# Optimization experiments

Hardware: AMD Instinct MI355X
Metric: run time of the kernel (lower is better)

## Reference

```python
import jax, jax.numpy as jnp
import numpy as np

N = 50000
E = 800000
F_IN = 128
HID = 32
NEG_SLOPE = 0.2  # PyG GATConv default


def _gat_layer(x, src, dst, W, a_src, a_dst, b, heads, out_c, concat, n_nodes):
    # Linear transform per head: [N, heads, out_c]
    h = (x @ W).reshape(n_nodes, heads, out_c)
    # Per-node attention logits per head
    al_src = jnp.einsum('nhc,hc->nh', h, a_src)  # source contribution
    al_dst = jnp.einsum('nhc,hc->nh', h, a_dst)  # destination contribution
    # Edge logits (message j=src -> i=dst), leaky relu
    e = jax.nn.leaky_relu(al_src[src] + al_dst[dst], NEG_SLOPE)  # [E', heads]
    # Segment softmax over incoming edges of each destination node
    m = jax.ops.segment_max(e, dst, num_segments=n_nodes)
    ex = jnp.exp(e - m[dst])
    denom = jax.ops.segment_sum(ex, dst, num_segments=n_nodes)
    alpha = ex / denom[dst]  # [E', heads]; self-loops guarantee denom > 0
    # Weighted scatter-aggregate of source features
    msg = h[src] * alpha[:, :, None]  # [E', heads, out_c]
    out = jax.ops.segment_sum(msg, dst, num_segments=n_nodes)  # [N, heads, out_c]
    out = out.reshape(n_nodes, heads * out_c) if concat else out.mean(axis=1)
    return out + b


def setup_inputs() -> dict:
    key = jax.random.key(0)
    ks = jax.random.split(key, 10)
    x = jax.random.normal(ks[0], (N, F_IN), dtype=jnp.float32)
    edge_index = jax.random.randint(ks[1], (2, E), 0, N, dtype=jnp.int64)
    s = 0.1
    return {
        'x': x,
        'edge_index': edge_index,
        'W1': jax.random.normal(ks[2], (F_IN, 4 * HID), dtype=jnp.float32) * s,
        'a_src1': jax.random.normal(ks[3], (4, HID), dtype=jnp.float32) * s,
        'a_dst1': jax.random.normal(ks[4], (4, HID), dtype=jnp.float32) * s,
        'b1': jnp.zeros((4 * HID,), jnp.float32),
        'W2': jax.random.normal(ks[5], (4 * HID, 2 * HID), dtype=jnp.float32) * s,
        'a_src2': jax.random.normal(ks[6], (2, HID), dtype=jnp.float32) * s,
        'a_dst2': jax.random.normal(ks[7], (2, HID), dtype=jnp.float32) * s,
        'b2': jnp.zeros((2 * HID,), jnp.float32),
        'W3': jax.random.normal(ks[8], (2 * HID, 1), dtype=jnp.float32) * s,
        'a_src3': jax.random.normal(ks[9], (1, 1), dtype=jnp.float32) * s,
        'a_dst3': jax.random.normal(jax.random.fold_in(key, 99), (1, 1), dtype=jnp.float32) * s,
        'b3': jnp.zeros((1,), jnp.float32),
    }


def reference(x, edge_index, W1, a_src1, a_dst1, b1, W2, a_src2, a_dst2, b2, W3, a_src3, a_dst3, b3):
    n = x.shape[0]
    # add_self_loops=True (PyG default)
    loop = jnp.arange(n, dtype=edge_index.dtype)
    src = jnp.concatenate([edge_index[0], loop])
    dst = jnp.concatenate([edge_index[1], loop])
    h = _gat_layer(x, src, dst, W1, a_src1, a_dst1, b1, 4, HID, True, n)
    h = jax.nn.elu(h)  # dropout is identity in eval mode
    h = _gat_layer(h, src, dst, W2, a_src2, a_dst2, b2, 2, HID, True, n)
    h = jax.nn.elu(h)
    out = _gat_layer(h, src, dst, W3, a_src3, a_dst3, b3, 1, 1, False, n)
    return out  # [N, 1]
```

## Files before the change

### kernel.cpp

```cpp
#include <hip/hip_runtime.h>
#include <hip/hip_fp16.h>
#include <math.h>

#define F_IN 128
constexpr int SB = 256;
constexpr float LOG2E = 1.4426950408889634f;
constexpr int CAP = 131072;
constexpr int CHUNK = 2048;
constexpr int NPAD = 50176;

__global__ void scan1(const int* __restrict__ degr, int* __restrict__ out,
                      int* __restrict__ bsums, int n, int selfN) {
    __shared__ int sm[SB];
    int i = blockIdx.x * SB + threadIdx.x;
    int v = 0;
    if (i < n) {
#pragma unroll
        for (int r = 0; r < 8; ++r) v += degr[r * NPAD + i];
        if (i < selfN) v += 1;
    }
    sm[threadIdx.x] = v;
    __syncthreads();
    for (int d = 1; d < SB; d <<= 1) {
        int t = (threadIdx.x >= d) ? sm[threadIdx.x - d] : 0;
        __syncthreads();
        sm[threadIdx.x] += t;
        __syncthreads();
    }
    if (i < n) out[i] = sm[threadIdx.x] - v;
    if (threadIdx.x == SB - 1) bsums[blockIdx.x] = sm[SB - 1];
}

__global__ void scan2(int* __restrict__ bsums, int nb) {
    __shared__ int sm[SB];
    int v = (threadIdx.x < nb) ? bsums[threadIdx.x] : 0;
    sm[threadIdx.x] = v;
    __syncthreads();
    for (int d = 1; d < SB; d <<= 1) {
        int t = (threadIdx.x >= d) ? sm[threadIdx.x - d] : 0;
        __syncthreads();
        sm[threadIdx.x] += t;
        __syncthreads();
    }
    if (threadIdx.x < nb) bsums[threadIdx.x] = sm[threadIdx.x] - v;
}

__global__ void scan3(int* __restrict__ off, int* __restrict__ cursor,
                      const int* __restrict__ bsums, int n, int ncur) {
    int i = blockIdx.x * SB + threadIdx.x;
    if (i < n) {
        int v = off[i] + bsums[blockIdx.x];
        off[i] = v;
        if (i < ncur) cursor[i] = v;
    }
}

template <int BN, int TN, int HEADS, typename AT>
__device__ __forceinline__ void gemm_dev(
    const AT* __restrict__ A, const float* __restrict__ B,
    const float* __restrict__ asrc, const float* __restrict__ adst,
    __half* __restrict__ C, float* __restrict__ als, float* __restrict__ ald,
    int M, int bid, char* smem) {
    constexpr int BM = 128, BK = 16, TM = 8, K = 128;
    float (*As)[BM + 4] = (float (*)[BM + 4])smem;
    float (*Bs)[BN] = (float (*)[BN])(smem + (size_t)BK * (BM + 4) * 4);
    const int tx = threadIdx.x, ty = threadIdx.y;
    const int tid = ty * 16 + tx;
    const int row0 = bid * BM;
    const int i0 = ty * TM;
    const int j0a = tx * 4;
    const int j0b = 64 + tx * 4;

    float acc[TM][TN];
#pragma unroll
    for (int m = 0; m < TM; ++m)
#pragma unroll
        for (int n = 0; n < TN; ++n) acc[m][n] = 0.f;

    const int ar = tid >> 1;
    const int ak = (tid & 1) * 8;
    int arow = row0 + ar;
    if (arow >= M) arow = M - 1;
    const AT* Aptr = A + (size_t)arow * K + ak;
    const int bk = tid >> 4;
    const int bc = (BN == 128) ? ((tid & 15) * 8) : ((tid & 15) * 4);

    for (int kc = 0; kc < K; kc += BK) {
        float av[8];
        if constexpr (sizeof(AT) == 4) {
            float4 a0 = *(const float4*)(Aptr + kc);
            float4 a1 = *(const float4*)(Aptr + kc + 4);
            av[0] = a0.x; av[1] = a0.y; av[2] = a0.z; av[3] = a0.w;
            av[4] = a1.x; av[5] = a1.y; av[6] = a1.z; av[7] = a1.w;
        } else {
            uint4 raw = *(const uint4*)(Aptr + kc);
            const __half2* hh = (const __half2*)&raw;
#pragma unroll
            for (int j = 0; j < 4; ++j) {
                float2 f = __half22float2(hh[j]);
                av[2 * j] = f.x;
                av[2 * j + 1] = f.y;
            }
        }
        float4 bv0, bv1;
        bv0 = *(const float4*)(B + (size_t)(kc + bk) * BN + bc);
        if constexpr (BN == 128) bv1 = *(const float4*)(B + (size_t)(kc + bk) * BN + bc + 4);
        __syncthreads();
#pragma unroll
        for (int j = 0; j < 8; ++j) As[ak + j][ar] = av[j];
        *(float4*)&Bs[bk][bc] = bv0;
        if constexpr (BN == 128) *(float4*)&Bs[bk][bc + 4] = bv1;
        __syncthreads();
#pragma unroll
        for (int kk = 0; kk < BK; ++kk) {
            float4 a4a = *(const float4*)&As[kk][i0];
            float4 a4b = *(const float4*)&As[kk][i0 + 4];
            float arr[TM] = {a4a.x, a4a.y, a4a.z, a4a.w, a4b.x, a4b.y, a4b.z, a4b.w};
            float br[TN];
            float4 b0 = *(const float4*)&Bs[kk][j0a];
            br[0] = b0.x; br[1] = b0.y; br[2] = b0.z; br[3] = b0.w;
            if constexpr (TN == 8) {
                float4 b1 = *(const float4*)&Bs[kk][j0b];
                br[4] = b1.x; br[5] = b1.y; br[6] = b1.z; br[7] = b1.w;
            }
#pragma unroll
            for (int m = 0; m < TM; ++m)
#pragma unroll
                for (int n = 0; n < TN; ++n) acc[m][n] += arr[m] * br[n];
        }
    }

#pragma unroll
    for (int m = 0; m < TM; ++m) {
        int row = row0 + i0 + m;
        bool ok = row < M;
        if constexpr (TN == 8) {
            if (ok) {
                alignas(8) __half2 pa[2], pb[2];
#pragma unroll
                for (int n2 = 0; n2 < 2; ++n2) {
                    pa[n2] = __floats2half2_rn(acc[m][2 * n2], acc[m][2 * n2 + 1]);
                    pb[n2] = __floats2half2_rn(acc[m][4 + 2 * n2], acc[m][5 + 2 * n2]);
                }
                *(uint2*)&C[(size_t)row * BN + j0a] = *(uint2*)pa;
                *(uint2*)&C[(size_t)row * BN + j0b] = *(uint2*)pb;
            }
            float psA = 0.f, pdA = 0.f, psB = 0.f, pdB = 0.f;
#pragma unroll
            for (int n = 0; n < 4; ++n) {
                psA += acc[m][n] * asrc[j0a + n];
                pdA += acc[m][n] * adst[j0a + n];
                psB += acc[m][n + 4] * asrc[j0b + n];
                pdB += acc[m][n + 4] * adst[j0b + n];
            }
#pragma unroll
            for (int msk = 1; msk < 8; msk <<= 1) {
                psA += __shfl_xor(psA, msk, 64);
                pdA += __shfl_xor(pdA, msk, 64);
                psB += __shfl_xor(psB, msk, 64);
                pdB += __shfl_xor(pdB, msk, 64);
            }
            if (ok && (tx & 7) == 0) {
                int hA = tx >> 3;
                als[row * HEADS + hA] = psA * LOG2E;
                ald[row * HEADS + hA] = pdA * LOG2E;
                als[row * HEADS + 2 + hA] = psB * LOG2E;
                ald[row * HEADS + 2 + hA] = pdB * LOG2E;
            }
        } else {
            if (ok) {
                alignas(8) __half2 ph[2];
#pragma unroll
                for (int n2 = 0; n2 < 2; ++n2)
                    ph[n2] = __floats2half2_rn(acc[m][2 * n2], acc[m][2 * n2 + 1]);
                *(uint2*)&C[(size_t)row * BN + j0a] = *(uint2*)ph;
            }
            float ps = 0.f, pd = 0.f;
#pragma unroll
            for (int n = 0; n < TN; ++n) {
                ps += acc[m][n] * asrc[j0a + n];
                pd += acc[m][n] * adst[j0a + n];
            }
#pragma unroll
            for (int msk = 1; msk < 8; msk <<= 1) {
                ps += __shfl_xor(ps, msk, 64);
                pd += __shfl_xor(pd, msk, 64);
            }
            if (ok && (tx & 7) == 0) {
                int h0 = tx >> 3;
                als[row * HEADS + h0] = ps * LOG2E;
                ald[row * HEADS + h0] = pd * LOG2E;
            }
        }
    }
}

__global__ __launch_bounds__(256) void gemm1_bucket(
    const float* __restrict__ A, const float* __restrict__ B,
    const float* __restrict__ asrc, const float* __restrict__ adst,
    __half* __restrict__ C, float* __restrict__ als, float* __restrict__ ald,
    int M, int gblk,
    const int* __restrict__ src, const int* __restrict__ dst,
    int* __restrict__ degr, int* __restrict__ bucketcur,
    int2* __restrict__ ebuf, int E, int nspan, int nchunk) {
    __shared__ __align__(16) char smem[16768];
    if ((int)blockIdx.x < gblk) {
        gemm_dev<128, 8, 4, float>(A, B, asrc, adst, C, als, ald, M, blockIdx.x, smem);
        return;
    }
    int cid = blockIdx.x - gblk;
    if (cid >= nchunk) return;
    int tid = threadIdx.y * 16 + threadIdx.x;
    int* degrep = degr + (blockIdx.x & 7) * NPAD;
    int2* stage = (int2*)smem;
    int* hist = (int*)(smem + CHUNK * 8);
    int* bbase = hist + 8;
    int* gbase = hist + 16;
    if (tid < 8) hist[tid] = 0;
    __syncthreads();
    int ebase = cid * CHUNK;
    int s[8], d[8], bk[8], slot[8];
#pragma unroll
    for (int k = 0; k < 8; ++k) {
        int e = ebase + k * 256 + tid;
        bool v = e < E;
        s[k] = v ? src[e] : 0;
        d[k] = v ? dst[e] : 0;
        bk[k] = -1;
        if (v) {
            bk[k] = d[k] / nspan;
            slot[k] = atomicAdd(&hist[bk[k]], 1);
            atomicAdd(&degrep[d[k]], 1);
        }
    }
    __syncthreads();
    if (tid == 0) {
        int run = 0;
#pragma unroll
        for (int b = 0; b < 8; ++b) { bbase[b] = run; run += hist[b]; }
    }
    if (tid < 8) gbase[tid] = atomicAdd(&bucketcur[tid], hist[tid]);
    __syncthreads();
#pragma unroll
    for (int k = 0; k < 8; ++k)
        if (bk[k] >= 0) stage[bbase[bk[k]] + slot[k]] = make_int2(s[k], d[k]);
    __syncthreads();
    for (int b = 0; b < 8; ++b) {
        int c0 = bbase[b], cN = hist[b];
        size_t g0 = (size_t)b * CAP + gbase[b];
        for (int j = tid; j < cN; j += 256) ebuf[g0 + j] = stage[c0 + j];
    }
}

__global__ void scatter_b(const int2* __restrict__ ebuf,
                          const int* __restrict__ bucketcur,
                          int* __restrict__ cursor, unsigned short* __restrict__ csr,
                          int N, int nspan, int spb) {
    int g = blockIdx.x & 7;
    int c = blockIdx.x >> 3;
    int tid = threadIdx.x;
    int cnt = bucketcur[g];
    const int2* eb = ebuf + (size_t)g * CAP;
    int stride = spb * 256;
    for (int i = c * 256 + tid; i < cnt; i += stride) {
        int2 e = eb[i];
        int p = atomicAdd(&cursor[e.y], 1);
        csr[p] = (unsigned short)e.x;
    }
    int r0 = g * nspan, r1 = r0 + nspan;
    if (r1 > N) r1 = N;
    for (int i = r0 + c * 256 + tid; i < r1; i += stride) {
        int p = atomicAdd(&cursor[i], 1);
        csr[p] = (unsigned short)i;
    }
}

template <int BN, int TN, int HEADS>
__global__ __launch_bounds__(256) void gemm_fused_h(
    const __half* __restrict__ A, const float* __restrict__ B,
    const float* __restrict__ asrc, const float* __restrict__ adst,
    __half* __restrict__ C, float* __restrict__ als, float* __restrict__ ald,
    int M) {
    __shared__ __align__(16) char smem[16 * 132 * 4 + 16 * BN * 4];
    gemm_dev<BN, TN, HEADS, __half>(A, B, asrc, adst, C, als, ald, M, blockIdx.x, smem);
}

__global__ void gat_agg_l1(const __half* __restrict__ h,
                           const float* __restrict__ als, const float* __restrict__ ald,
                           const float* __restrict__ bias,
                           const int* __restrict__ off,
                           const unsigned short* __restrict__ csr,
                           __half* __restrict__ out, int n) {
    int wid = (blockIdx.x * blockDim.x + threadIdx.x) >> 6;
    int lane = threadIdx.x & 63;
    if (wid >= n) return;
    const int g = lane >> 4;
    const int q = lane & 15;
    const int hd = q >> 2;
    float ad = ald[wid * 4 + hd];
    int e0 = off[wid], e1 = off[wid + 1];
    const __half* hq = h + q * 8;

    float acc[8] = {0.f, 0.f, 0.f, 0.f, 0.f, 0.f, 0.f, 0.f};
    float D = 0.f;

    auto LD = [&](int ebase, uint4& h4, float& al) {
        int ee = ebase + g;
        int ie = (ee < e1) ? ee : e1 - 1;
        int s = csr[ie];
        float av = als[s * 4 + hd];
        al = (ee < e1) ? av : -1e30f;
        h4 = *(const uint4*)(hq + (size_t)s * 128);
    };
    auto PROC = [&](const uint4& h4, float al) {
        float lg = al + ad;
        lg = fmaxf(lg, 0.2f * lg);
        float exv = exp2f(lg);
        D += exv;
        const __half2* hh = (const __half2*)&h4;
#pragma unroll
        for (int i = 0; i < 4; ++i) {
            float2 f = __half22float2(hh[i]);
            acc[2 * i] = fmaf(exv, f.x, acc[2 * i]);
            acc[2 * i + 1] = fmaf(exv, f.y, acc[2 * i + 1]);
        }
    };

    uint4 hA, hB;
    float alA, alB;
    LD(e0, hA, alA);
    LD(e0 + 4, hB, alB);
    int e = e0;
    for (; e + 8 < e1; e += 8) {
        uint4 nA, nB;
        float nalA, nalB;
        LD(e + 8, nA, nalA);
        LD(e + 12, nB, nalB);
        PROC(hA, alA);
        PROC(hB, alB);
        hA = nA; alA = nalA;
        hB = nB; alB = nalB;
    }
    PROC(hA, alA);
    PROC(hB, alB);

#pragma unroll
    for (int i = 0; i < 8; ++i) {
        acc[i] += __shfl_xor(acc[i], 16, 64);
        acc[i] += __shfl_xor(acc[i], 32, 64);
    }
    D += __shfl_xor(D, 16, 64);
    D += __shfl_xor(D, 32, 64);

    if (g == 0) {
        float inv = 1.f / D;
        alignas(16) __half2 ph[4];
#pragma unroll
        for (int i = 0; i < 4; ++i) {
            float2 bv = ((const float2*)bias)[q * 4 + i];
            float vx = acc[2 * i] * inv + bv.x;
            float vy = acc[2 * i + 1] * inv + bv.y;
            vx = vx > 0.f ? vx : (__expf(vx) - 1.f);
            vy = vy > 0.f ? vy : (__expf(vy) - 1.f);
            ph[i] = __floats2half2_rn(vx, vy);
        }
        *(uint4*)(out + (size_t)wid * 128 + q * 8) = *(uint4*)ph;
    }
}

__global__ void gat_agg_l2(const __half* __restrict__ h,
                           const float* __restrict__ als, const float* __restrict__ ald,
                           const float* __restrict__ bias,
                           const int* __restrict__ off,
                           const unsigned short* __restrict__ csr,
                           const float* __restrict__ W3, const float* __restrict__ as3,
                           const float* __restrict__ ad3, float2* __restrict__ hs,
                           float* __restrict__ ald3, int n) {
    int wid = (blockIdx.x * blockDim.x + threadIdx.x) >> 6;
    int lane = threadIdx.x & 63;
    if (wid >= n) return;
    const int g = lane >> 3;
    const int q = lane & 7;
    const int hd = q >> 2;
    float ad = ald[wid * 2 + hd];
    int e0 = off[wid], e1 = off[wid + 1];
    const __half* hq = h + q * 8;

    float acc[8] = {0.f, 0.f, 0.f, 0.f, 0.f, 0.f, 0.f, 0.f};
    float D = 0.f;

    auto LD = [&](int ebase, uint4& h4, float& al) {
        int ee = ebase + g;
        int ie = (ee < e1) ? ee : e1 - 1;
        int s = csr[ie];
        float av = als[s * 2 + hd];
        al = (ee < e1) ? av : -1e30f;
        h4 = *(const uint4*)(hq + (size_t)s * 64);
    };
    auto PROC = [&](const uint4& h4, float al) {
        float lg = al + ad;
        lg = fmaxf(lg, 0.2f * lg);
        float exv = exp2f(lg);
        D += exv;
        const __half2* hh = (const __half2*)&h4;
#pragma unroll
        for (int i = 0; i < 4; ++i) {
            float2 f = __half22float2(hh[i]);
            acc[2 * i] = fmaf(exv, f.x, acc[2 * i]);
            acc[2 * i + 1] = fmaf(exv, f.y, acc[2 * i + 1]);
        }
    };

    uint4 hA, hB;
    float alA, alB;
    LD(e0, hA, alA);
    LD(e0 + 8, hB, alB);
    int e = e0;
    for (; e + 16 < e1; e += 16) {
        uint4 nA, nB;
        float nalA, nalB;
        LD(e + 16, nA, nalA);
        LD(e + 24, nB, nalB);
        PROC(hA, alA);
        PROC(hB, alB);
        hA = nA; alA = nalA;
        hB = nB; alB = nalB;
    }
    PROC(hA, alA);
    PROC(hB, alB);

#pragma unroll
    for (int i = 0; i < 8; ++i) {
        acc[i] += __shfl_xor(acc[i], 8, 64);
        acc[i] += __shfl_xor(acc[i], 16, 64);
        acc[i] += __shfl_xor(acc[i], 32, 64);
    }
    D += __shfl_xor(D, 8, 64);
    D += __shfl_xor(D, 16, 64);
    D += __shfl_xor(D, 32, 64);

    float inv = 1.f / D;
    float r = 0.f;
#pragma unroll
    for (int i = 0; i < 8; ++i) {
        float v = acc[i] * inv + bias[q * 8 + i];
        v = v > 0.f ? v : (__expf(v) - 1.f);
        r = fmaf(v, W3[q * 8 + i], r);
    }
#pragma unroll
    for (int msk = 1; msk < 8; msk <<= 1) r += __shfl_xor(r, msk, 64);
    if (lane == 0) {
        hs[wid] = make_float2(r, r * as3[0] * LOG2E);
        ald3[wid] = r * ad3[0] * LOG2E;
    }
}

__global__ void gat_agg1(const float2* __restrict__ hs, const float* __restrict__ ald3,
                         const float* __restrict__ bias,
                         const int* __restrict__ off,
                         const unsigned short* __restrict__ csr,
                         float* __restrict__ out, int n) {
    int i = blockIdx.x * blockDim.x + threadIdx.x;
    if (i >= n) return;
    float ad = ald3[i];
    int e0 = off[i], e1 = off[i + 1];
    float S = 0.f, D = 0.f;
    float2 g[2];
    float valid[2];
#pragma unroll
    for (int p = 0; p < 2; ++p) {
        int ee = e0 + p;
        int ie = (ee < e1) ? ee : e1 - 1;
        int s = csr[ie];
        g[p] = hs[s];
        valid[p] = (ee < e1) ? 0.f : -1e30f;
    }
    int e = e0;
    for (; e + 2 < e1; e += 2) {
#pragma unroll
        for (int p = 0; p < 2; ++p) {
            int ee = e + 2 + p;
            int ie = (ee < e1) ? ee : e1 - 1;
            int s = csr[ie];
            float2 ng = hs[s];
            float nvalid = (ee < e1) ? 0.f : -1e30f;
            float lg = g[p].y + ad + valid[p];
            lg = fmaxf(lg, 0.2f * lg);
            float exv = exp2f(lg);
            D += exv;
            S = fmaf(exv, g[p].x, S);
            g[p] = ng;
            valid[p] = nvalid;
        }
    }
#pragma unroll
    for (int p = 0; p < 2; ++p) {
        float lg = g[p].y + ad + valid[p];
        lg = fmaxf(lg, 0.2f * lg);
        float exv = exp2f(lg);
        D += exv;
        S = fmaf(exv, g[p].x, S);
    }
    out[i] = S / D + bias[0];
}

extern "C" void kernel_launch(void* const* d_in, const int* in_sizes, int n_in,
                              void* d_out, int out_size, void* d_ws, size_t ws_size,
                              hipStream_t stream) {
    const float* x   = (const float*)d_in[0];
    const int*   ei  = (const int*)d_in[1];
    const float* W1  = (const float*)d_in[2];
    const float* as1 = (const float*)d_in[3];
    const float* ad1 = (const float*)d_in[4];
    const float* b1  = (const float*)d_in[5];
    const float* W2  = (const float*)d_in[6];
    const float* as2 = (const float*)d_in[7];
    const float* ad2 = (const float*)d_in[8];
    const float* b2  = (const float*)d_in[9];
    const float* W3  = (const float*)d_in[10];
    const float* as3 = (const float*)d_in[11];
    const float* ad3 = (const float*)d_in[12];
    const float* b3  = (const float*)d_in[13];
    float* out = (float*)d_out;

    const int N = in_sizes[0] / F_IN;
    const int E = in_sizes[1] / 2;
    const int ET = E + N;

    char* w = (char*)d_ws;
    size_t o = 0;
    auto alloc = [&](size_t bytes) -> void* {
        void* p = w + o;
        o += (bytes + 255) & ~(size_t)255;
        return p;
    };
    __half* hbuf = (__half*)alloc((size_t)N * 128 * 2);
    __half* a1   = (__half*)alloc((size_t)N * 128 * 2);
    float2* hs   = (float2*)alloc((size_t)N * 8);
    float* als  = (float*)alloc((size_t)N * 4 * 4);
    float* ald  = (float*)alloc((size_t)N * 4 * 4);
    float* ald3 = (float*)alloc((size_t)N * 4);
    int* degr   = (int*)alloc((size_t)8 * NPAD * 4);
    int* bucketcur = (int*)alloc(8 * 4);
    int* off    = (int*)alloc((size_t)(N + 1) * 4);
    int* cursor = (int*)alloc((size_t)N * 4);
    int* bsums  = (int*)alloc(1024);
    unsigned short* csr = (unsigned short*)alloc((size_t)ET * 2);
    int2* ebuf  = (int2*)alloc((size_t)8 * CAP * 8);

    __half* h2 = hbuf;

    const int* esrc = ei;
    const int* edst = ei + E;
    const int nspan = (N + 7) >> 3;
    const int nchunk = (E + CHUNK - 1) / CHUNK;

    hipMemsetAsync(degr, 0, (size_t)8 * NPAD * 4, stream);
    hipMemsetAsync(bucketcur, 0, 8 * 4, stream);

    const int gblk = (N + 127) / 128;

    gemm1_bucket<<<gblk + nchunk, dim3(16, 16), 0, stream>>>(
        x, W1, as1, ad1, hbuf, als, ald, N, gblk,
        esrc, edst, degr, bucketcur, ebuf, E, nspan, nchunk);

    int n1 = N + 1;
    int nb = (n1 + SB - 1) / SB;
    scan1<<<nb, SB, 0, stream>>>(degr, off, bsums, n1, N);
    scan2<<<1, SB, 0, stream>>>(bsums, nb);
    scan3<<<nb, SB, 0, stream>>>(off, cursor, bsums, n1, N);

    {
        const int spb = 64;
        scatter_b<<<8 * spb, 256, 0, stream>>>(ebuf, bucketcur, cursor, csr, N, nspan, spb);
    }

    gat_agg_l1<<<(N * 64 + 255) / 256, 256, 0, stream>>>(
        hbuf, als, ald, b1, off, csr, a1, N);

    gemm_fused_h<64, 4, 2><<<gblk, dim3(16, 16), 0, stream>>>(
        a1, W2, as2, ad2, h2, als, ald, N);
    gat_agg_l2<<<(N * 64 + 255) / 256, 256, 0, stream>>>(
        h2, als, ald, b2, off, csr, W3, as3, ad3, hs, ald3, N);

    gat_agg1<<<(N + 255) / 256, 256, 0, stream>>>(hs, ald3, b3, off, csr, out, N);
}
```

Baseline: 180.8 us.

## Replace FP32 SIMT GEMMs with FP16 MFMA GEMMs using pre-transposed weights

Both dense transforms (layer 1 and layer 2) move from a scalar FP32 register-tiled GEMM to MFMA 16x16x32 f16 instructions. A small prep kernel converts and transposes W1/W2 into padded FP16 layouts that are staged whole in LDS, and each wave computes a 16-row strip. Layer-1 input x is cast to FP16 on the fly, which lowers precision. Block size changes to 1D 256 with 64 rows per block, and the scatter launch width is halved.

```diff
diff --git a/kernel.cpp b/kernel.cpp
--- a/kernel.cpp
+++ b/kernel.cpp
@@ -8,6 +8,25 @@
 constexpr int CAP = 131072;
 constexpr int CHUNK = 2048;
 constexpr int NPAD = 50176;
+constexpr int PK = 136;
+
+typedef _Float16 h8 __attribute__((ext_vector_type(8)));
+typedef float f4 __attribute__((ext_vector_type(4)));
+
+__global__ void prep_w(const float* __restrict__ W1, const float* __restrict__ W2,
+                       _Float16* __restrict__ w1t, _Float16* __restrict__ w2t) {
+    int i = blockIdx.x * 256 + threadIdx.x;
+    if (i < 128 * 128) {
+        int k = i >> 7, n = i & 127;
+        w1t[n * PK + k] = (_Float16)W1[i];
+    } else {
+        int j = i - 128 * 128;
+        if (j < 128 * 64) {
+            int k = j >> 6, n = j & 63;
+            w2t[n * PK + k] = (_Float16)W2[j];
+        }
+    }
+}
 
 __global__ void scan1(const int* __restrict__ degr, int* __restrict__ out,
                       int* __restrict__ bsums, int n, int selfN) {
@@ -55,162 +74,96 @@
     }
 }
 
-template <int BN, int TN, int HEADS, typename AT>
-__device__ __forceinline__ void gemm_dev(
-    const AT* __restrict__ A, const float* __restrict__ B,
+template <int NT, int HEADS, typename AT>
+__device__ __forceinline__ void gemm_mfma(
+    const AT* __restrict__ A, const _Float16* __restrict__ Wt,
     const float* __restrict__ asrc, const float* __restrict__ adst,
     __half* __restrict__ C, float* __restrict__ als, float* __restrict__ ald,
-    int M, int bid, char* smem) {
-    constexpr int BM = 128, BK = 16, TM = 8, K = 128;
-    float (*As)[BM + 4] = (float (*)[BM + 4])smem;
-    float (*Bs)[BN] = (float (*)[BN])(smem + (size_t)BK * (BM + 4) * 4);
-    const int tx = threadIdx.x, ty = threadIdx.y;
-    const int tid = ty * 16 + tx;
-    const int row0 = bid * BM;
-    const int i0 = ty * TM;
-    const int j0a = tx * 4;
-    const int j0b = 64 + tx * 4;
-
-    float acc[TM][TN];
-#pragma unroll
-    for (int m = 0; m < TM; ++m)
-#pragma unroll
-        for (int n = 0; n < TN; ++n) acc[m][n] = 0.f;
-
-    const int ar = tid >> 1;
-    const int ak = (tid & 1) * 8;
-    int arow = row0 + ar;
+    int M, int bid, _Float16* lds) {
+    constexpr int N = NT * 16;
+    const int tid = threadIdx.x;
+    constexpr int HW = N * PK;
+    for (int i = tid * 8; i < HW; i += 256 * 8)
+        *(uint4*)&lds[i] = *(const uint4*)&Wt[i];
+    __syncthreads();
+    const int w = tid >> 6;
+    const int lane = tid & 63;
+    const int l15 = lane & 15, lg = lane >> 4;
+    const int strip = bid * 64 + w * 16;
+    int arow = strip + l15;
     if (arow >= M) arow = M - 1;
-    const AT* Aptr = A + (size_t)arow * K + ak;
-    const int bk = tid >> 4;
-    const int bc = (BN == 128) ? ((tid & 15) * 8) : ((tid & 15) * 4);
-
-    for (int kc = 0; kc < K; kc += BK) {
-        float av[8];
+
+    f4 acc[NT];
+#pragma unroll
+    for (int t = 0; t < NT; ++t) acc[t] = (f4){0.f, 0.f, 0.f, 0.f};
+
+#pragma unroll
+    for (int c = 0; c < 4; ++c) {
+        h8 a;
         if constexpr (sizeof(AT) == 4) {
-            float4 a0 = *(const float4*)(Aptr + kc);
-            float4 a1 = *(const float4*)(Aptr + kc + 4);
-            av[0] = a0.x; av[1] = a0.y; av[2] = a0.z; av[3] = a0.w;
-            av[4] = a1.x; av[5] = a1.y; av[6] = a1.z; av[7] = a1.w;
+            const float* ap = (const float*)A + (size_t)arow * 128 + c * 32 + lg * 8;
+            float4 a0 = *(const float4*)ap;
+            float4 a1 = *(const float4*)(ap + 4);
+            a[0] = (_Float16)a0.x; a[1] = (_Float16)a0.y;
+            a[2] = (_Float16)a0.z; a[3] = (_Float16)a0.w;
+            a[4] = (_Float16)a1.x; a[5] = (_Float16)a1.y;
+            a[6] = (_Float16)a1.z; a[7] = (_Float16)a1.w;
         } else {
-            uint4 raw = *(const uint4*)(Aptr + kc);
-            const __half2* hh = (const __half2*)&raw;
-#pragma unroll
-            for (int j = 0; j < 4; ++j) {
-                float2 f = __half22float2(hh[j]);
-                av[2 * j] = f.x;
-                av[2 * j + 1] = f.y;
+            a = *(const h8*)((const _Float16*)A + (size_t)arow * 128 + c * 32 + lg * 8);
+        }
+#pragma unroll
+        for (int t = 0; t < NT; ++t) {
+            h8 b = *(const h8*)(lds + (t * 16 + l15) * PK + c * 32 + lg * 8);
+            acc[t] = __builtin_amdgcn_mfma_f32_16x16x32_f16(a, b, acc[t], 0, 0, 0);
+        }
+    }
+
+    const int rbase = strip + lg * 4;
+#pragma unroll
+    for (int r = 0; r < 4; ++r) {
+        int orow = rbase + r;
+        bool ok = orow < M;
+        if (ok) {
+#pragma unroll
+            for (int t = 0; t < NT; ++t)
+                C[(size_t)orow * N + t * 16 + l15] = __float2half(acc[t][r]);
+        }
+#pragma unroll
+        for (int h = 0; h < HEADS; ++h) {
+            float ps = acc[2 * h][r] * asrc[32 * h + l15]
+                     + acc[2 * h + 1][r] * asrc[32 * h + 16 + l15];
+            float pd = acc[2 * h][r] * adst[32 * h + l15]
+                     + acc[2 * h + 1][r] * adst[32 * h + 16 + l15];
+#pragma unroll
+            for (int m = 1; m < 16; m <<= 1) {
+                ps += __shfl_xor(ps, m, 64);
+                pd += __shfl_xor(pd, m, 64);
             }
-        }
-        float4 bv0, bv1;
-        bv0 = *(const float4*)(B + (size_t)(kc + bk) * BN + bc);
-        if constexpr (BN == 128) bv1 = *(const float4*)(B + (size_t)(kc + bk) * BN + bc + 4);
-        __syncthreads();
-#pragma unroll
-        for (int j = 0; j < 8; ++j) As[ak + j][ar] = av[j];
-        *(float4*)&Bs[bk][bc] = bv0;
-        if constexpr (BN == 128) *(float4*)&Bs[bk][bc + 4] = bv1;
-        __syncthreads();
-#pragma unroll
-        for (int kk = 0; kk < BK; ++kk) {
-            float4 a4a = *(const float4*)&As[kk][i0];
-            float4 a4b = *(const float4*)&As[kk][i0 + 4];
-            float arr[TM] = {a4a.x, a4a.y, a4a.z, a4a.w, a4b.x, a4b.y, a4b.z, a4b.w};
-            float br[TN];
-            float4 b0 = *(const float4*)&Bs[kk][j0a];
-            br[0] = b0.x; br[1] = b0.y; br[2] = b0.z; br[3] = b0.w;
-            if constexpr (TN == 8) {
-                float4 b1 = *(const float4*)&Bs[kk][j0b];
-                br[4] = b1.x; br[5] = b1.y; br[6] = b1.z; br[7] = b1.w;
+            if (ok && l15 == 0) {
+                als[orow * HEADS + h] = ps * LOG2E;
+                ald[orow * HEADS + h] = pd * LOG2E;
             }
-#pragma unroll
-            for (int m = 0; m < TM; ++m)
-#pragma unroll
-                for (int n = 0; n < TN; ++n) acc[m][n] += arr[m] * br[n];
-        }
-    }
-
-#pragma unroll
-    for (int m = 0; m < TM; ++m) {
-        int row = row0 + i0 + m;
-        bool ok = row < M;
-        if constexpr (TN == 8) {
-            if (ok) {
-                alignas(8) __half2 pa[2], pb[2];
-#pragma unroll
-                for (int n2 = 0; n2 < 2; ++n2) {
-                    pa[n2] = __floats2half2_rn(acc[m][2 * n2], acc[m][2 * n2 + 1]);
-                    pb[n2] = __floats2half2_rn(acc[m][4 + 2 * n2], acc[m][5 + 2 * n2]);
-                }
-                *(uint2*)&C[(size_t)row * BN + j0a] = *(uint2*)pa;
-                *(uint2*)&C[(size_t)row * BN + j0b] = *(uint2*)pb;
-            }
-            float psA = 0.f, pdA = 0.f, psB = 0.f, pdB = 0.f;
-#pragma unroll
-            for (int n = 0; n < 4; ++n) {
-                psA += acc[m][n] * asrc[j0a + n];
-                pdA += acc[m][n] * adst[j0a + n];
-                psB += acc[m][n + 4] * asrc[j0b + n];
-                pdB += acc[m][n + 4] * adst[j0b + n];
-            }
-#pragma unroll
-            for (int msk = 1; msk < 8; msk <<= 1) {
-                psA += __shfl_xor(psA, msk, 64);
-                pdA += __shfl_xor(pdA, msk, 64);
-                psB += __shfl_xor(psB, msk, 64);
-                pdB += __shfl_xor(pdB, msk, 64);
-            }
-            if (ok && (tx & 7) == 0) {
-                int hA = tx >> 3;
-                als[row * HEADS + hA] = psA * LOG2E;
-                ald[row * HEADS + hA] = pdA * LOG2E;
-                als[row * HEADS + 2 + hA] = psB * LOG2E;
-                ald[row * HEADS + 2 + hA] = pdB * LOG2E;
-            }
-        } else {
-            if (ok) {
-                alignas(8) __half2 ph[2];
-#pragma unroll
-                for (int n2 = 0; n2 < 2; ++n2)
-                    ph[n2] = __floats2half2_rn(acc[m][2 * n2], acc[m][2 * n2 + 1]);
-                *(uint2*)&C[(size_t)row * BN + j0a] = *(uint2*)ph;
-            }
-            float ps = 0.f, pd = 0.f;
-#pragma unroll
-            for (int n = 0; n < TN; ++n) {
-                ps += acc[m][n] * asrc[j0a + n];
-                pd += acc[m][n] * adst[j0a + n];
-            }
-#pragma unroll
-            for (int msk = 1; msk < 8; msk <<= 1) {
-                ps += __shfl_xor(ps, msk, 64);
-                pd += __shfl_xor(pd, msk, 64);
-            }
-            if (ok && (tx & 7) == 0) {
-                int h0 = tx >> 3;
-                als[row * HEADS + h0] = ps * LOG2E;
-                ald[row * HEADS + h0] = pd * LOG2E;
-            }
         }
     }
 }
 
 __global__ __launch_bounds__(256) void gemm1_bucket(
-    const float* __restrict__ A, const float* __restrict__ B,
+    const float* __restrict__ A, const _Float16* __restrict__ w1t,
     const float* __restrict__ asrc, const float* __restrict__ adst,
     __half* __restrict__ C, float* __restrict__ als, float* __restrict__ ald,
     int M, int gblk,
     const int* __restrict__ src, const int* __restrict__ dst,
     int* __restrict__ degr, int* __restrict__ bucketcur,
     int2* __restrict__ ebuf, int E, int nspan, int nchunk) {
-    __shared__ __align__(16) char smem[16768];
+    __shared__ __align__(16) char smem[128 * PK * 2];
     if ((int)blockIdx.x < gblk) {
-        gemm_dev<128, 8, 4, float>(A, B, asrc, adst, C, als, ald, M, blockIdx.x, smem);
+        gemm_mfma<8, 4, float>(A, w1t, asrc, adst, C, als, ald, M, blockIdx.x,
+                               (_Float16*)smem);
         return;
     }
     int cid = blockIdx.x - gblk;
     if (cid >= nchunk) return;
-    int tid = threadIdx.y * 16 + threadIdx.x;
+    int tid = threadIdx.x;
     int* degrep = degr + (blockIdx.x & 7) * NPAD;
     int2* stage = (int2*)smem;
     int* hist = (int*)(smem + CHUNK * 8);
@@ -250,6 +203,16 @@
         size_t g0 = (size_t)b * CAP + gbase[b];
         for (int j = tid; j < cN; j += 256) ebuf[g0 + j] = stage[c0 + j];
     }
+}
+
+__global__ __launch_bounds__(256) void gemm2_mfma(
+    const _Float16* __restrict__ A, const _Float16* __restrict__ w2t,
+    const float* __restrict__ asrc, const float* __restrict__ adst,
+    __half* __restrict__ C, float* __restrict__ als, float* __restrict__ ald,
+    int M) {
+    __shared__ __align__(16) char smem[64 * PK * 2];
+    gemm_mfma<4, 2, _Float16>(A, w2t, asrc, adst, C, als, ald, M, blockIdx.x,
+                              (_Float16*)smem);
 }
 
 __global__ void scatter_b(const int2* __restrict__ ebuf,
@@ -273,16 +236,6 @@
         int p = atomicAdd(&cursor[i], 1);
         csr[p] = (unsigned short)i;
     }
-}
-
-template <int BN, int TN, int HEADS>
-__global__ __launch_bounds__(256) void gemm_fused_h(
-    const __half* __restrict__ A, const float* __restrict__ B,
-    const float* __restrict__ asrc, const float* __restrict__ adst,
-    __half* __restrict__ C, float* __restrict__ als, float* __restrict__ ald,
-    int M) {
-    __shared__ __align__(16) char smem[16 * 132 * 4 + 16 * BN * 4];
-    gemm_dev<BN, TN, HEADS, __half>(A, B, asrc, adst, C, als, ald, M, blockIdx.x, smem);
 }
 
 __global__ void gat_agg_l1(const __half* __restrict__ h,
@@ -546,6 +499,8 @@
     int* cursor = (int*)alloc((size_t)N * 4);
     int* bsums  = (int*)alloc(1024);
     unsigned short* csr = (unsigned short*)alloc((size_t)ET * 2);
+    _Float16* w1t = (_Float16*)alloc(128 * PK * 2);
+    _Float16* w2t = (_Float16*)alloc(64 * PK * 2);
     int2* ebuf  = (int2*)alloc((size_t)8 * CAP * 8);
 
     __half* h2 = hbuf;
@@ -558,10 +513,12 @@
     hipMemsetAsync(degr, 0, (size_t)8 * NPAD * 4, stream);
     hipMemsetAsync(bucketcur, 0, 8 * 4, stream);
 
-    const int gblk = (N + 127) / 128;
-
-    gemm1_bucket<<<gblk + nchunk, dim3(16, 16), 0, stream>>>(
-        x, W1, as1, ad1, hbuf, als, ald, N, gblk,
+    prep_w<<<(128 * 128 + 128 * 64 + 255) / 256, 256, 0, stream>>>(W1, W2, w1t, w2t);
+
+    const int gblk = (N + 63) / 64;
+
+    gemm1_bucket<<<gblk + nchunk, 256, 0, stream>>>(
+        x, w1t, as1, ad1, hbuf, als, ald, N, gblk,
         esrc, edst, degr, bucketcur, ebuf, E, nspan, nchunk);
 
     int n1 = N + 1;
@@ -571,15 +528,15 @@
     scan3<<<nb, SB, 0, stream>>>(off, cursor, bsums, n1, N);
 
     {
-        const int spb = 64;
+        const int spb = 32;
         scatter_b<<<8 * spb, 256, 0, stream>>>(ebuf, bucketcur, cursor, csr, N, nspan, spb);
     }
 
     gat_agg_l1<<<(N * 64 + 255) / 256, 256, 0, stream>>>(
         hbuf, als, ald, b1, off, csr, a1, N);
 
-    gemm_fused_h<64, 4, 2><<<gblk, dim3(16, 16), 0, stream>>>(
-        a1, W2, as2, ad2, h2, als, ald, N);
+    gemm2_mfma<<<gblk, 256, 0, stream>>>(
+        (const _Float16*)a1, w2t, as2, ad2, h2, als, ald, N);
     gat_agg_l2<<<(N * 64 + 255) / 256, 256, 0, stream>>>(
         h2, als, ald, b2, off, csr, W3, as3, ad3, hs, ald3, N);
 
```

Result: faster. 177.0 us, median of 2 (-2.1%).
